# Optimization experiments

Hardware: AMD Instinct MI355X
Metric: run time of the kernel (lower is better)

The kernel has to match this reference:

```python
import jax, jax.numpy as jnp
import numpy as np

EPS = 1e-12  # matches torch F.normalize eps

def _l2norm(v, axis):
    n = jnp.linalg.norm(v, axis=axis, keepdims=True)
    return v / jnp.maximum(n, EPS)

def setup_inputs() -> dict:
    key = jax.random.key(0)
    k1, k2 = jax.random.split(key)
    x = jax.random.normal(k1, (16, 512, 64, 64), dtype=jnp.float32)
    mem = jax.random.normal(k2, (1024, 512), dtype=jnp.float32)
    memory = _l2norm(mem, axis=1)  # buffer initialized normalized, as in __init__
    return {"x": x, "memory": memory}

def reference(x, memory):
    B, C, H, W = x.shape
    feat = x.transpose(0, 2, 3, 1).reshape(-1, C)          # [N, C], N=B*H*W
    feat_norm = _l2norm(feat, axis=1)                       # [N, C]
    mem_norm = _l2norm(memory, axis=1)                      # [K, C]
    sim = feat_norm @ mem_norm.T                            # [N, K] cosine sims
    attn = jax.nn.softmax(sim, axis=1)                      # [N, K]
    recon = attn @ mem_norm                                 # [N, C]
    recon = recon.reshape(B, H, W, C).transpose(0, 3, 1, 2) # [B, C, H, W]
    match_map = attn.max(axis=1).reshape(B, H, W)           # [B, H, W]
    return recon, match_map
```

## Files before the change

### kernel.cpp

```cpp
#include <hip/hip_runtime.h>

#define C_DIM 512
#define K_MEM 1024

typedef __attribute__((ext_vector_type(8))) short short8;
typedef __attribute__((ext_vector_type(16))) float f32x16;
typedef __attribute__((ext_vector_type(4))) unsigned int u32x4;

#define LGKM0()  asm volatile("s_waitcnt lgkmcnt(0)" ::: "memory")
#define BAR()    { asm volatile("" ::: "memory"); __builtin_amdgcn_s_barrier(); asm volatile("" ::: "memory"); }

#define GLOAD16(dst, addr, imm) \
    asm volatile("global_load_dwordx4 %0, %1, off offset:%c2" \
                 : "=v"(dst) : "v"(addr), "n"(imm))

#define WAITV(N) do { asm volatile("s_waitcnt vmcnt(%c0)" :: "n"(N) : "memory"); \
                      __builtin_amdgcn_sched_barrier(0); } while (0)

__device__ __forceinline__ unsigned short f2bf(float f) {
    unsigned int u = __builtin_bit_cast(unsigned int, f);
    unsigned int r = (u + 0x7fffu + ((u >> 16) & 1u)) >> 16;
    return (unsigned short)r;
}

__device__ __forceinline__ f32x16 mfma32(short8 a, short8 b, f32x16 c) {
    return __builtin_amdgcn_mfma_f32_32x32x16_bf16(a, b, c, 0, 0, 0);
}

__global__ __launch_bounds__(256)
void prep_norm(const float* __restrict__ mem, unsigned short* __restrict__ Mn) {
    int k = blockIdx.x, t = threadIdx.x;
    const float* row = mem + (size_t)k * C_DIM;
    float2 v = *reinterpret_cast<const float2*>(row + 2 * t);
    float ss = v.x * v.x + v.y * v.y;
#pragma unroll
    for (int off = 32; off >= 1; off >>= 1) ss += __shfl_xor(ss, off);
    __shared__ float wp[4];
    if ((t & 63) == 0) wp[t >> 6] = ss;
    __syncthreads();
    float tot = wp[0] + wp[1] + wp[2] + wp[3];
    float rn = 1.0f / fmaxf(sqrtf(tot), 1e-12f);
    unsigned int pk = (unsigned int)f2bf(v.x * rn) | ((unsigned int)f2bf(v.y * rn) << 16);
    *reinterpret_cast<unsigned int*>(Mn + (size_t)k * C_DIM + 2 * t) = pk;
}

__global__ __launch_bounds__(256)
void prep_transpose(const unsigned short* __restrict__ Mn, unsigned short* __restrict__ MnT) {
    __shared__ unsigned short tl[64][72];
    int t = threadIdx.x;
    int bk = blockIdx.x & 15, bc = blockIdx.x >> 4;
    int k0 = bk * 64, c0 = bc * 64;
    {
        int kr = t >> 2, gc = (t & 3) * 16;
        const u32x4* src = reinterpret_cast<const u32x4*>(Mn + (size_t)(k0 + kr) * C_DIM + c0 + gc);
        u32x4 a = src[0], b = src[1];
        *reinterpret_cast<u32x4*>(&tl[kr][gc]) = a;
        *reinterpret_cast<u32x4*>(&tl[kr][gc + 8]) = b;
    }
    __syncthreads();
    {
        int cr = t >> 2, gk = (t & 3) * 16;
        unsigned int ow[8];
#pragma unroll
        for (int j = 0; j < 8; ++j)
            ow[j] = (unsigned int)tl[gk + 2 * j][cr] | ((unsigned int)tl[gk + 2 * j + 1][cr] << 16);
        unsigned int* dst = reinterpret_cast<unsigned int*>(MnT + (size_t)(c0 + cr) * K_MEM + k0 + gk);
#pragma unroll
        for (int j = 0; j < 8; ++j) dst[j] = ow[j];
    }
}

__global__ __launch_bounds__(512)
__attribute__((amdgpu_waves_per_eu(2, 2)))
void fused_attn(const float* __restrict__ x,
                const unsigned short* __restrict__ Mn,
                const unsigned short* __restrict__ MnT,
                float* __restrict__ recon,
                float* __restrict__ match) {
    __shared__ alignas(16) char FnB[65536];
    __shared__ alignas(16) char PldsB[2 * 32768];
    __shared__ float Zinv[64], rnormS[64];

    const int t = threadIdx.x;
    const int bid = blockIdx.x;
    const int b = bid >> 6, h = bid & 63;
    const int lane = t & 63, wv = t >> 6;
    const int l31 = lane & 31, l5 = lane >> 5;
    const int ko = wv;
    const int cb = wv * 64;

    {
        float* normpart = (float*)PldsB;
        const int w = lane, cg = wv;
        const float* xp = x + (size_t)b * 2097152 + (size_t)(cg * 64) * 4096 + (size_t)h * 64 + w;
        float xv[64];
#pragma unroll
        for (int i = 0; i < 64; ++i) xv[i] = xp[(size_t)i * 4096];
        float ss = 0.f;
#pragma unroll
        for (int i = 0; i < 64; ++i) ss += xv[i] * xv[i];
        normpart[w * 9 + cg] = ss;
        __syncthreads();
        if (t < 64) {
            float s = 0.f;
#pragma unroll
            for (int j = 0; j < 8; ++j) s += normpart[t * 9 + j];
            rnormS[t] = 1.0f / fmaxf(sqrtf(s), 1e-12f);
        }
        __syncthreads();
        float rn = rnormS[w];
        char* fnrow = FnB + w * 1024;
#pragma unroll
        for (int j = 0; j < 8; ++j) {
            u32x4 pk4;
#pragma unroll
            for (int p = 0; p < 4; ++p) {
                float v0 = xv[j * 8 + 2 * p] * rn;
                float v1 = xv[j * 8 + 2 * p + 1] * rn;
                pk4[p] = (unsigned int)f2bf(v0) | ((unsigned int)f2bf(v1) << 16);
            }
            int gs = (cg * 8 + j) ^ (w & 31);
            *(u32x4*)(fnrow + (gs << 4)) = pk4;
        }
    }
    __syncthreads();

    f32x16 acc3[2][2];
#pragma unroll
    for (int i = 0; i < 2; ++i)
#pragma unroll
        for (int j = 0; j < 2; ++j)
#pragma unroll
            for (int r = 0; r < 16; ++r) acc3[i][j][r] = 0.f;

    float regZ[2] = {0.f, 0.f};
    float regM[2] = {-3.0e38f, -3.0e38f};

    const char* fnR0 = FnB + l31 * 1024;
    const char* fnR1 = FnB + (32 + l31) * 1024;

#pragma unroll 1
    for (int kt = 0; kt < 4; ++kt) {
        const char* aG = (const char*)Mn + ((size_t)(kt * 256 + ko * 32 + l31) << 10) + (l5 << 4);

        u32x4 afb[2][4];
        GLOAD16(afb[0][0], aG, 0);
        GLOAD16(afb[0][1], aG, 32);
        GLOAD16(afb[0][2], aG, 64);
        GLOAD16(afb[0][3], aG, 96);

        f32x16 acc1[2];
#pragma unroll
        for (int j = 0; j < 2; ++j)
#pragma unroll
            for (int r = 0; r < 16; ++r) acc1[j][r] = 0.f;

#pragma unroll
        for (int g = 0; g < 8; ++g) {
            if (g < 7) {
#pragma unroll
                for (int s = 0; s < 4; ++s)
                    GLOAD16(afb[(g + 1) & 1][s], aG, ((g + 1) * 4 + s) * 32);
                WAITV(4);
            } else {
                WAITV(0);
            }
#pragma unroll
            for (int s = 0; s < 4; ++s) {
                const int st = g * 4 + s;
                const int gsw = (((st << 1) | l5) ^ l31) << 4;
                short8 b0 = *(const short8*)(fnR0 + gsw);
                short8 b1 = *(const short8*)(fnR1 + gsw);
                short8 av = __builtin_bit_cast(short8, afb[g & 1][s]);
                acc1[0] = mfma32(av, b0, acc1[0]);
                acc1[1] = mfma32(av, b1, acc1[1]);
            }
        }

        const char* aG2a = (const char*)MnT + ((size_t)(cb + l31) << 11) + ((size_t)kt << 9) + (l5 << 4);
        const char* aG2b = aG2a + 65536;
        u32x4 a2b[2][4];
        GLOAD16(a2b[0][0], aG2a, 0);
        GLOAD16(a2b[0][1], aG2b, 0);
        GLOAD16(a2b[0][2], aG2a, 32);
        GLOAD16(a2b[0][3], aG2b, 32);

        unsigned int P32[2][8];
#pragma unroll
        for (int nt = 0; nt < 2; ++nt) {
            float s0 = 0.f, m0 = -3.0e38f;
#pragma unroll
            for (int j = 0; j < 8; ++j) {
                float a0 = acc1[nt][2 * j], a1 = acc1[nt][2 * j + 1];
                m0 = fmaxf(m0, fmaxf(a0, a1));
                float e0 = __expf(a0), e1 = __expf(a1);
                P32[nt][j] = (unsigned int)f2bf(e0) | ((unsigned int)f2bf(e1) << 16);
                s0 += e0 + e1;
            }
            s0 += __shfl_xor(s0, 32);
            m0 = fmaxf(m0, __shfl_xor(m0, 32));
            regZ[nt] += s0;
            regM[nt] = fmaxf(regM[nt], m0);
        }

        char* Pb = PldsB + (kt & 1) * 32768;
#pragma unroll
        for (int nt = 0; nt < 2; ++nt) {
            const int n = nt * 32 + l31;
            char* prow = Pb + n * 512;
#pragma unroll
            for (int jp = 0; jp < 4; ++jp) {
                const int gk = ko * 4 + jp;
                uint2 v;
                v.x = P32[nt][2 * jp];
                v.y = P32[nt][2 * jp + 1];
                *(uint2*)(prow + ((gk ^ (n & 31)) << 4) + 8 * l5) = v;
            }
        }
        LGKM0(); BAR();

#pragma unroll
        for (int g = 0; g < 8; ++g) {
            if (g < 7) {
#pragma unroll
                for (int u = 0; u < 2; ++u) {
                    GLOAD16(a2b[(g + 1) & 1][u * 2 + 0], aG2a, ((g + 1) * 2 + u) * 32);
                    GLOAD16(a2b[(g + 1) & 1][u * 2 + 1], aG2b, ((g + 1) * 2 + u) * 32);
                }
                WAITV(4);
            } else {
                WAITV(0);
            }
#pragma unroll
            for (int u = 0; u < 2; ++u) {
                const int ks = g * 2 + u;
                const int gsw = (((ks << 1) | l5) ^ l31) << 4;
                short8 bp0 = *(const short8*)(Pb + l31 * 512 + gsw);
                short8 bp1 = *(const short8*)(Pb + (32 + l31) * 512 + gsw);
                short8 a0 = __builtin_bit_cast(short8, a2b[g & 1][u * 2 + 0]);
                short8 a1 = __builtin_bit_cast(short8, a2b[g & 1][u * 2 + 1]);
                acc3[0][0] = mfma32(a0, bp0, acc3[0][0]);
                acc3[0][1] = mfma32(a0, bp1, acc3[0][1]);
                acc3[1][0] = mfma32(a1, bp0, acc3[1][0]);
                acc3[1][1] = mfma32(a1, bp1, acc3[1][1]);
            }
        }
    }

    {
        float* pS = (float*)FnB;
        float* pM = (float*)(FnB + 2048);
        if (l5 == 0) {
            pS[ko * 64 + l31] = regZ[0];
            pS[ko * 64 + 32 + l31] = regZ[1];
            pM[ko * 64 + l31] = regM[0];
            pM[ko * 64 + 32 + l31] = regM[1];
        }
        LGKM0(); BAR();
        if (t < 64) {
            float s = 0.f, m = -3.0e38f;
#pragma unroll
            for (int k8 = 0; k8 < 8; ++k8) {
                s += pS[k8 * 64 + t];
                m = fmaxf(m, pM[k8 * 64 + t]);
            }
            float zi = 1.0f / s;
            Zinv[t] = zi;
            match[(size_t)bid * 64 + t] = __expf(m) * zi;
        }
        LGKM0(); BAR();
    }

    const float zi0 = Zinv[l31], zi1 = Zinv[32 + l31];
    float* rbase = recon + (size_t)b * 2097152 + (size_t)h * 64;
#pragma unroll
    for (int ct = 0; ct < 2; ++ct) {
#pragma unroll
        for (int r = 0; r < 16; ++r) {
            const int c = cb + ct * 32 + (r & 3) + 8 * (r >> 2) + 4 * l5;
            float* rp = rbase + (size_t)c * 4096;
            rp[l31] = acc3[ct][0][r] * zi0;
            rp[32 + l31] = acc3[ct][1][r] * zi1;
        }
    }
}

extern "C" void kernel_launch(void* const* d_in, const int* in_sizes, int n_in,
                              void* d_out, int out_size, void* d_ws, size_t ws_size,
                              hipStream_t stream) {
    (void)in_sizes; (void)n_in; (void)out_size;
    if (ws_size < (size_t)2 * 1024 * 1024) return;

    const float* x = (const float*)d_in[0];
    const float* mem = (const float*)d_in[1];
    float* recon = (float*)d_out;
    float* match = recon + (size_t)16 * 512 * 64 * 64;
    unsigned short* Mn = (unsigned short*)d_ws;
    unsigned short* MnT = Mn + (size_t)K_MEM * C_DIM;

    prep_norm<<<dim3(K_MEM), dim3(256), 0, stream>>>(mem, Mn);
    prep_transpose<<<dim3(128), dim3(256), 0, stream>>>(Mn, MnT);
    fused_attn<<<dim3(1024), dim3(512), 0, stream>>>(x, Mn, MnT, recon, match);
}
```

Baseline: 290.9 us.

## Split fused attention into normalize, GEMM1+exp, stats and GEMM2 kernels

Replaces the single fused kernel with a multi-kernel pipeline when the workspace is large enough. The stages are an x-normalization kernel writing bf16 features, a tiled 16x16 MFMA GEMM that stores exp(sim) as a bf16 P matrix plus partial sums and maxes, a stats reduction kernel, and a second tiled GEMM producing recon. The aim is better MFMA tile utilization and occupancy using LDS-staged global_load_lds tiles. The cost is materializing a 128 MB P matrix and extra kernel launches, which adds substantial HBM traffic. The fused kernel is kept as a fallback when the workspace is too small.

```diff
diff --git a/kernel.cpp b/kernel.cpp
--- a/kernel.cpp
+++ b/kernel.cpp
@@ -4,16 +4,17 @@
 #define K_MEM 1024
 
 typedef __attribute__((ext_vector_type(8))) short short8;
+typedef __attribute__((ext_vector_type(4))) float f32x4;
 typedef __attribute__((ext_vector_type(16))) float f32x16;
 typedef __attribute__((ext_vector_type(4))) unsigned int u32x4;
 
 #define LGKM0()  asm volatile("s_waitcnt lgkmcnt(0)" ::: "memory")
+#define VM0()    asm volatile("s_waitcnt vmcnt(0)" ::: "memory")
 #define BAR()    { asm volatile("" ::: "memory"); __builtin_amdgcn_s_barrier(); asm volatile("" ::: "memory"); }
 
 #define GLOAD16(dst, addr, imm) \
     asm volatile("global_load_dwordx4 %0, %1, off offset:%c2" \
                  : "=v"(dst) : "v"(addr), "n"(imm))
-
 #define WAITV(N) do { asm volatile("s_waitcnt vmcnt(%c0)" :: "n"(N) : "memory"); \
                       __builtin_amdgcn_sched_barrier(0); } while (0)
 
@@ -23,8 +24,17 @@
     return (unsigned short)r;
 }
 
+__device__ __forceinline__ f32x4 mfma16(short8 a, short8 b, f32x4 c) {
+    return __builtin_amdgcn_mfma_f32_16x16x32_bf16(a, b, c, 0, 0, 0);
+}
 __device__ __forceinline__ f32x16 mfma32(short8 a, short8 b, f32x16 c) {
     return __builtin_amdgcn_mfma_f32_32x32x16_bf16(a, b, c, 0, 0, 0);
+}
+
+__device__ __forceinline__ void gl_lds16(const void* g, void* l) {
+    __builtin_amdgcn_global_load_lds(
+        (const __attribute__((address_space(1))) unsigned int*)g,
+        (__attribute__((address_space(3))) unsigned int*)l, 16, 0, 0);
 }
 
 __global__ __launch_bounds__(256)
@@ -71,6 +81,256 @@
 }
 
 __global__ __launch_bounds__(512)
+void normx_kernel(const float* __restrict__ x, unsigned short* __restrict__ Fn) {
+    __shared__ alignas(16) char FnB[65536];
+    __shared__ float normpart[64][9];
+    __shared__ float rnormS[64];
+    const int t = threadIdx.x, bid = blockIdx.x;
+    const int b = bid >> 6, h = bid & 63;
+    const int lane = t & 63, wv = t >> 6;
+    const int w = lane, cg = wv;
+    const float* xp = x + (size_t)b * 2097152 + (size_t)(cg * 64) * 4096 + (size_t)h * 64 + w;
+    float xv[64];
+#pragma unroll
+    for (int i = 0; i < 64; ++i) xv[i] = xp[(size_t)i * 4096];
+    float ss = 0.f;
+#pragma unroll
+    for (int i = 0; i < 64; ++i) ss += xv[i] * xv[i];
+    normpart[w][cg] = ss;
+    __syncthreads();
+    if (t < 64) {
+        float s = 0.f;
+#pragma unroll
+        for (int j = 0; j < 8; ++j) s += normpart[t][j];
+        rnormS[t] = 1.0f / fmaxf(sqrtf(s), 1e-12f);
+    }
+    __syncthreads();
+    float rn = rnormS[w];
+    char* fnrow = FnB + w * 1024;
+#pragma unroll
+    for (int j = 0; j < 8; ++j) {
+        u32x4 pk4;
+#pragma unroll
+        for (int p = 0; p < 4; ++p) {
+            float v0 = xv[j * 8 + 2 * p] * rn;
+            float v1 = xv[j * 8 + 2 * p + 1] * rn;
+            pk4[p] = (unsigned int)f2bf(v0) | ((unsigned int)f2bf(v1) << 16);
+        }
+        int gs = (cg * 8 + j) ^ (w & 31);
+        *(u32x4*)(fnrow + (gs << 4)) = pk4;
+    }
+    __syncthreads();
+    const int r = t >> 3;
+    char* orow = (char*)(Fn + (size_t)(bid * 64 + r) * C_DIM);
+#pragma unroll
+    for (int p = 0; p < 8; ++p) {
+        int gl = p * 8 + (t & 7);
+        u32x4 v = *(const u32x4*)(FnB + r * 1024 + ((gl ^ (r & 31)) << 4));
+        *(u32x4*)(orow + gl * 16) = v;
+    }
+}
+
+__device__ __forceinline__ void stage_tile(const char* g0, size_t rowBytes, int col0,
+                                           char* lds0, int wv, int lane) {
+#pragma unroll
+    for (int j = 0; j < 4; ++j) {
+        const int chunk = wv * 4 + j;
+        const int r = chunk * 8 + (lane >> 3);
+        const int gs = (lane & 7) ^ (r & 7);
+        const char* src = g0 + (size_t)r * rowBytes + col0 + gs * 16;
+        gl_lds16(src, lds0 + chunk * 1024);
+    }
+}
+
+#define FRAG(base, r, gk) (*(const short8*)((base) + (r) * 128 + ((((gk)) ^ ((r) & 7)) << 4)))
+
+__global__ __launch_bounds__(256, 3)
+void gemm1_kernel(const unsigned short* __restrict__ Fn, const unsigned short* __restrict__ Mn,
+                  unsigned short* __restrict__ P, float* __restrict__ Zp, float* __restrict__ Mp) {
+    __shared__ alignas(16) char LDSU[34816];
+    __shared__ float zS[128][2], zM[128][2];
+    char* As = LDSU;
+    char* Bs = LDSU + 16384;
+
+    const int wg = (blockIdx.x & 7) * 512 + (blockIdx.x >> 3);
+    const int mt = wg >> 3, nt = wg & 7;
+    const int m0 = mt * 128, n0 = nt * 128;
+    const int t = threadIdx.x, lane = t & 63, wv = t >> 6;
+    const int wm = wv >> 1, wn = wv & 1;
+    const int l15 = lane & 15, l4 = lane >> 4;
+
+    const char* Ag = (const char*)Fn + (size_t)m0 * 1024;
+    const char* Bg = (const char*)Mn + (size_t)n0 * 1024;
+
+    f32x4 acc[4][4];
+#pragma unroll
+    for (int i = 0; i < 4; ++i)
+#pragma unroll
+        for (int j = 0; j < 4; ++j) acc[i][j] = (f32x4){0.f, 0.f, 0.f, 0.f};
+
+#pragma unroll 1
+    for (int kt = 0; kt < 8; ++kt) {
+        stage_tile(Ag, 1024, kt * 128, As, wv, lane);
+        stage_tile(Bg, 1024, kt * 128, Bs, wv, lane);
+        VM0(); BAR();
+#pragma unroll
+        for (int ks = 0; ks < 2; ++ks) {
+            short8 af[4], bfr[4];
+#pragma unroll
+            for (int i = 0; i < 4; ++i) {
+                af[i]  = FRAG(As, wm * 64 + i * 16 + l15, ks * 4 + l4);
+                bfr[i] = FRAG(Bs, wn * 64 + i * 16 + l15, ks * 4 + l4);
+            }
+#pragma unroll
+            for (int mf = 0; mf < 4; ++mf)
+#pragma unroll
+                for (int nf = 0; nf < 4; ++nf)
+                    acc[mf][nf] = mfma16(af[mf], bfr[nf], acc[mf][nf]);
+        }
+        LGKM0(); BAR();
+    }
+
+    float zsum[4][4], zmax[4][4];
+#pragma unroll
+    for (int mf = 0; mf < 4; ++mf)
+#pragma unroll
+        for (int r = 0; r < 4; ++r) { zsum[mf][r] = 0.f; zmax[mf][r] = 0.f; }
+#pragma unroll
+    for (int mf = 0; mf < 4; ++mf)
+#pragma unroll
+        for (int nf = 0; nf < 4; ++nf)
+#pragma unroll
+            for (int r = 0; r < 4; ++r) {
+                float e = __expf(acc[mf][nf][r]);
+                acc[mf][nf][r] = e;
+                zsum[mf][r] += e;
+                zmax[mf][r] = fmaxf(zmax[mf][r], e);
+            }
+#pragma unroll
+    for (int off = 1; off < 16; off <<= 1)
+#pragma unroll
+        for (int mf = 0; mf < 4; ++mf)
+#pragma unroll
+            for (int r = 0; r < 4; ++r) {
+                zsum[mf][r] += __shfl_xor(zsum[mf][r], off);
+                zmax[mf][r] = fmaxf(zmax[mf][r], __shfl_xor(zmax[mf][r], off));
+            }
+    if (l15 == 0) {
+#pragma unroll
+        for (int mf = 0; mf < 4; ++mf)
+#pragma unroll
+            for (int r = 0; r < 4; ++r) {
+                int row = wm * 64 + mf * 16 + l4 * 4 + r;
+                zS[row][wn] = zsum[mf][r];
+                zM[row][wn] = zmax[mf][r];
+            }
+    }
+    char* Pscr = LDSU;
+#pragma unroll
+    for (int mf = 0; mf < 4; ++mf)
+#pragma unroll
+        for (int nf = 0; nf < 4; ++nf)
+#pragma unroll
+            for (int r = 0; r < 4; ++r) {
+                int row = wm * 64 + mf * 16 + l4 * 4 + r;
+                int col = wn * 64 + nf * 16 + l15;
+                *(unsigned short*)(Pscr + row * 272 + col * 2) = f2bf(acc[mf][nf][r]);
+            }
+    LGKM0(); BAR();
+    if (t < 128) {
+        float zq = zS[t][0] + zS[t][1];
+        float mq = fmaxf(zM[t][0], zM[t][1]);
+        Zp[(size_t)(m0 + t) * 8 + nt] = zq;
+        Mp[(size_t)(m0 + t) * 8 + nt] = mq;
+    }
+#pragma unroll
+    for (int p = 0; p < 8; ++p) {
+        int r = (t >> 4) + p * 16;
+        u32x4 v = *(const u32x4*)(Pscr + r * 272 + (t & 15) * 16);
+        *(u32x4*)((char*)P + (size_t)(m0 + r) * 2048 + n0 * 2 + (t & 15) * 16) = v;
+    }
+}
+
+__global__ __launch_bounds__(256)
+void stats_kernel(const float* __restrict__ Zp, const float* __restrict__ Mp,
+                  float* __restrict__ Zinv, float* __restrict__ match) {
+    int i = blockIdx.x * 256 + threadIdx.x;
+    f32x4 a = *(const f32x4*)(Zp + (size_t)i * 8);
+    f32x4 b = *(const f32x4*)(Zp + (size_t)i * 8 + 4);
+    float s = (a[0] + a[1] + a[2] + a[3]) + (b[0] + b[1] + b[2] + b[3]);
+    f32x4 c = *(const f32x4*)(Mp + (size_t)i * 8);
+    f32x4 d = *(const f32x4*)(Mp + (size_t)i * 8 + 4);
+    float m = fmaxf(fmaxf(fmaxf(c[0], c[1]), fmaxf(c[2], c[3])),
+                    fmaxf(fmaxf(d[0], d[1]), fmaxf(d[2], d[3])));
+    float zi = 1.0f / s;
+    Zinv[i] = zi;
+    match[i] = m * zi;
+}
+
+__global__ __launch_bounds__(256, 3)
+void gemm2_kernel(const unsigned short* __restrict__ P, const unsigned short* __restrict__ MnT,
+                  const float* __restrict__ Zinv, float* __restrict__ recon) {
+    __shared__ alignas(16) char As[16384];
+    __shared__ alignas(16) char Bs[16384];
+    __shared__ float zinvS[128];
+
+    const int wg = (blockIdx.x & 7) * 256 + (blockIdx.x >> 3);
+    const int mt = wg >> 2, nt = wg & 3;
+    const int m0 = mt * 128, n0 = nt * 128;
+    const int t = threadIdx.x, lane = t & 63, wv = t >> 6;
+    const int wm = wv >> 1, wn = wv & 1;
+    const int l15 = lane & 15, l4 = lane >> 4;
+
+    if (t < 128) zinvS[t] = Zinv[m0 + t];
+
+    const char* Ag = (const char*)P + (size_t)m0 * 2048;
+    const char* Bg = (const char*)MnT + (size_t)n0 * 2048;
+
+    f32x4 acc[4][4];
+#pragma unroll
+    for (int i = 0; i < 4; ++i)
+#pragma unroll
+        for (int j = 0; j < 4; ++j) acc[i][j] = (f32x4){0.f, 0.f, 0.f, 0.f};
+
+#pragma unroll 1
+    for (int kt = 0; kt < 16; ++kt) {
+        stage_tile(Ag, 2048, kt * 128, As, wv, lane);
+        stage_tile(Bg, 2048, kt * 128, Bs, wv, lane);
+        VM0(); BAR();
+#pragma unroll
+        for (int ks = 0; ks < 2; ++ks) {
+            short8 af[4], bfr[4];
+#pragma unroll
+            for (int i = 0; i < 4; ++i) {
+                af[i]  = FRAG(As, wm * 64 + i * 16 + l15, ks * 4 + l4);
+                bfr[i] = FRAG(Bs, wn * 64 + i * 16 + l15, ks * 4 + l4);
+            }
+#pragma unroll
+            for (int mf = 0; mf < 4; ++mf)
+#pragma unroll
+                for (int nf = 0; nf < 4; ++nf)
+                    acc[mf][nf] = mfma16(af[mf], bfr[nf], acc[mf][nf]);
+        }
+        LGKM0(); BAR();
+    }
+
+    const int b = m0 >> 12;
+    const int inb0 = m0 & 4095;
+#pragma unroll
+    for (int mf = 0; mf < 4; ++mf) {
+        f32x4 zv = *(const f32x4*)(&zinvS[wm * 64 + mf * 16 + l4 * 4]);
+#pragma unroll
+        for (int nf = 0; nf < 4; ++nf) {
+            f32x4 v = acc[mf][nf];
+            v[0] *= zv[0]; v[1] *= zv[1]; v[2] *= zv[2]; v[3] *= zv[3];
+            int c = n0 + wn * 64 + nf * 16 + l15;
+            int inb = inb0 + wm * 64 + mf * 16 + l4 * 4;
+            *(f32x4*)(recon + (size_t)b * 2097152 + (size_t)c * 4096 + inb) = v;
+        }
+    }
+}
+
+__global__ __launch_bounds__(512)
 __attribute__((amdgpu_waves_per_eu(2, 2)))
 void fused_attn(const float* __restrict__ x,
                 const unsigned short* __restrict__ Mn,
@@ -135,26 +395,22 @@
 
     float regZ[2] = {0.f, 0.f};
     float regM[2] = {-3.0e38f, -3.0e38f};
-
     const char* fnR0 = FnB + l31 * 1024;
     const char* fnR1 = FnB + (32 + l31) * 1024;
 
 #pragma unroll 1
     for (int kt = 0; kt < 4; ++kt) {
         const char* aG = (const char*)Mn + ((size_t)(kt * 256 + ko * 32 + l31) << 10) + (l5 << 4);
-
         u32x4 afb[2][4];
         GLOAD16(afb[0][0], aG, 0);
         GLOAD16(afb[0][1], aG, 32);
         GLOAD16(afb[0][2], aG, 64);
         GLOAD16(afb[0][3], aG, 96);
-
         f32x16 acc1[2];
 #pragma unroll
         for (int j = 0; j < 2; ++j)
 #pragma unroll
             for (int r = 0; r < 16; ++r) acc1[j][r] = 0.f;
-
 #pragma unroll
         for (int g = 0; g < 8; ++g) {
             if (g < 7) {
@@ -176,7 +432,6 @@
                 acc1[1] = mfma32(av, b1, acc1[1]);
             }
         }
-
         const char* aG2a = (const char*)MnT + ((size_t)(cb + l31) << 11) + ((size_t)kt << 9) + (l5 << 4);
         const char* aG2b = aG2a + 65536;
         u32x4 a2b[2][4];
@@ -184,7 +439,6 @@
         GLOAD16(a2b[0][1], aG2b, 0);
         GLOAD16(a2b[0][2], aG2a, 32);
         GLOAD16(a2b[0][3], aG2b, 32);
-
         unsigned int P32[2][8];
 #pragma unroll
         for (int nt = 0; nt < 2; ++nt) {
@@ -202,7 +456,6 @@
             regZ[nt] += s0;
             regM[nt] = fmaxf(regM[nt], m0);
         }
-
         char* Pb = PldsB + (kt & 1) * 32768;
 #pragma unroll
         for (int nt = 0; nt < 2; ++nt) {
@@ -218,7 +471,6 @@
             }
         }
         LGKM0(); BAR();
-
 #pragma unroll
         for (int g = 0; g < 8; ++g) {
             if (g < 7) {
@@ -246,7 +498,6 @@
             }
         }
     }
-
     {
         float* pS = (float*)FnB;
         float* pM = (float*)(FnB + 2048);
@@ -270,7 +521,6 @@
         }
         LGKM0(); BAR();
     }
-
     const float zi0 = Zinv[l31], zi1 = Zinv[32 + l31];
     float* rbase = recon + (size_t)b * 2097152 + (size_t)h * 64;
 #pragma unroll
@@ -295,10 +545,25 @@
     const float* mem = (const float*)d_in[1];
     float* recon = (float*)d_out;
     float* match = recon + (size_t)16 * 512 * 64 * 64;
-    unsigned short* Mn = (unsigned short*)d_ws;
-    unsigned short* MnT = Mn + (size_t)K_MEM * C_DIM;
+    char* ws = (char*)d_ws;
+    unsigned short* Mn = (unsigned short*)ws;
+    unsigned short* MnT = (unsigned short*)(ws + 1048576);
 
     prep_norm<<<dim3(K_MEM), dim3(256), 0, stream>>>(mem, Mn);
     prep_transpose<<<dim3(128), dim3(256), 0, stream>>>(Mn, MnT);
-    fused_attn<<<dim3(1024), dim3(512), 0, stream>>>(x, Mn, MnT, recon, match);
-}
+
+    const size_t NEED = 207880192ull;
+    if (ws_size >= NEED) {
+        unsigned short* Fn = (unsigned short*)(ws + 2097152);
+        unsigned short* P  = (unsigned short*)(ws + 69206016);
+        float* Zp   = (float*)(ws + 203423744);
+        float* Mp   = (float*)(ws + 205520896);
+        float* Zi   = (float*)(ws + 207618048);
+        normx_kernel<<<dim3(1024), dim3(512), 0, stream>>>(x, Fn);
+        gemm1_kernel<<<dim3(4096), dim3(256), 0, stream>>>(Fn, Mn, P, Zp, Mp);
+        stats_kernel<<<dim3(256), dim3(256), 0, stream>>>(Zp, Mp, Zi, match);
+        gemm2_kernel<<<dim3(2048), dim3(256), 0, stream>>>(P, MnT, Zi, recon);
+    } else {
+        fused_attn<<<dim3(1024), dim3(512), 0, stream>>>(x, Mn, MnT, recon, match);
+    }
+}
```

Result: faster. 250.1 us (-14.0%).
